# Kernel tuning notes

Hardware: AMD Instinct MI355X
Metric: run time of the kernel (lower is better)

The kernel has to match this reference:

```python
import jax, jax.numpy as jnp
import numpy as np

HIDDEN = 2048
N_HEADS = 32
N_KV_HEADS = 8
HEAD_DIM = HIDDEN // N_HEADS  # 64
N_GROUPS = N_HEADS // N_KV_HEADS  # 4
B, S = 1, 2048
NEG_INF = -1e9


def setup_inputs() -> dict:
    key = jax.random.key(0)
    k1, k2, k3, k4, k5 = jax.random.split(key, 5)
    hidden_states = jax.random.normal(k1, (B, S, HIDDEN), dtype=jnp.float32)
    # additive causal mask [B,1,S,S]
    causal = jnp.triu(jnp.full((S, S), NEG_INF, dtype=jnp.float32), k=1)
    attention_mask = jnp.broadcast_to(causal[None, None], (B, 1, S, S))
    position_ids = jnp.broadcast_to(jnp.arange(S, dtype=jnp.int32)[None], (B, S))
    scale = 0.02
    Wq = jax.random.normal(k2, (HIDDEN, N_HEADS * HEAD_DIM), dtype=jnp.float32) * scale
    Wk = jax.random.normal(k3, (HIDDEN, N_KV_HEADS * HEAD_DIM), dtype=jnp.float32) * scale
    Wv = jax.random.normal(k4, (HIDDEN, N_KV_HEADS * HEAD_DIM), dtype=jnp.float32) * scale
    Wo = jax.random.normal(k5, (HIDDEN, HIDDEN), dtype=jnp.float32) * scale
    return {"hidden_states": hidden_states, "attention_mask": attention_mask,
            "position_ids": position_ids, "Wq": Wq, "Wk": Wk, "Wv": Wv, "Wo": Wo}


def _rotate_half(x):
    x1, x2 = jnp.split(x, 2, axis=-1)
    return jnp.concatenate([-x2, x1], axis=-1)


def _rope_tables(kv_seq_len):
    inv_freq = 1.0 / (10000.0 ** (jnp.arange(0, HEAD_DIM, 2, dtype=jnp.float32) / HEAD_DIM))
    pos = jnp.arange(kv_seq_len, dtype=jnp.float32)
    freqs = pos[:, None] * inv_freq[None, :]          # [S, HD/2]
    emb = jnp.concatenate([freqs, freqs], axis=-1)    # [S, HD]
    return jnp.sin(emb), jnp.cos(emb)


def reference(hidden_states, attention_mask, position_ids, Wq, Wk, Wv, Wo):
    b, s, _ = hidden_states.shape
    q = (hidden_states @ Wq).reshape(b, s, N_HEADS, HEAD_DIM).transpose(0, 2, 1, 3)
    k = (hidden_states @ Wk).reshape(b, s, N_KV_HEADS, HEAD_DIM).transpose(0, 2, 1, 3)
    v = (hidden_states @ Wv).reshape(b, s, N_KV_HEADS, HEAD_DIM).transpose(0, 2, 1, 3)

    sin, cos = _rope_tables(s)
    cos_p = cos[position_ids][:, None]  # [B,1,S,HD]
    sin_p = sin[position_ids][:, None]
    q = q * cos_p + _rotate_half(q) * sin_p
    k = k * cos_p + _rotate_half(k) * sin_p

    # GQA: repeat_interleave kv heads along head axis
    k = jnp.repeat(k, N_GROUPS, axis=1)  # [B,H,S,HD]
    v = jnp.repeat(v, N_GROUPS, axis=1)

    q = q / jnp.sqrt(jnp.asarray(HEAD_DIM, q.dtype))
    scores = jnp.einsum('bhqd,bhkd->bhqk', q, k) + attention_mask
    attn = jax.nn.softmax(scores, axis=-1)
    out = jnp.einsum('bhqk,bhkd->bhqd', attn, v)
    out = out.transpose(0, 2, 1, 3).reshape(b, s, HIDDEN)
    return out @ Wo
```

## Files before the change

kernel.cpp:

```cpp
#include <hip/hip_runtime.h>
#include <hip/hip_bf16.h>

#define S_LEN 2048
#define HID 2048

typedef __attribute__((ext_vector_type(8))) short s16x8;
typedef __attribute__((ext_vector_type(4))) float f32x4;
typedef unsigned short u16;

__device__ __forceinline__ u16 f2bf(float f) {
  __hip_bfloat16 h = __float2bfloat16(f);
  return __builtin_bit_cast(u16, h);
}
__device__ __forceinline__ float bf2f(u16 u) {
  __hip_bfloat16 h = __builtin_bit_cast(__hip_bfloat16, u);
  return __bfloat162float(h);
}

#define GLD16(dst, src)                                                        \
  __builtin_amdgcn_global_load_lds(                                            \
      (__attribute__((address_space(1))) void*)(src),                          \
      (__attribute__((address_space(3))) void*)(dst), 16, 0, 0)

__global__ __launch_bounds__(256) void f2b_kernel(const float* __restrict__ in,
                                                  u16* __restrict__ outp, int n4) {
  int idx = blockIdx.x * 256 + threadIdx.x;
  if (idx >= n4) return;
  float4 v = *((const float4*)in + idx);
  ushort4 o;
  o.x = f2bf(v.x); o.y = f2bf(v.y); o.z = f2bf(v.z); o.w = f2bf(v.w);
  *((ushort4*)outp + idx) = o;
}

__global__ __launch_bounds__(256) void wtrans_kernel(const float* __restrict__ in,
                                                     u16* __restrict__ outp, int K, int N) {
  __shared__ u16 tile[32][33];
  int n0 = blockIdx.x * 32, k0 = blockIdx.y * 32;
  int tx = threadIdx.x & 31, ty = threadIdx.x >> 5;
#pragma unroll
  for (int r = 0; r < 4; ++r) {
    int row = ty + r * 8;
    tile[row][tx] = f2bf(in[(size_t)(k0 + row) * N + n0 + tx]);
  }
  __syncthreads();
#pragma unroll
  for (int r = 0; r < 4; ++r) {
    int row = ty + r * 8;
    outp[(size_t)(n0 + row) * K + k0 + tx] = tile[tx][row];
  }
}

__global__ __launch_bounds__(256) void wtransQKV_kernel(const float* __restrict__ Wq,
                                                        const float* __restrict__ Wk,
                                                        const float* __restrict__ Wv,
                                                        u16* __restrict__ outp) {
  __shared__ u16 tile[32][33];
  int n0g = blockIdx.x * 32, k0 = blockIdx.y * 32;
  const float* src;
  int n0, N;
  if (n0g < 2048)      { src = Wq; n0 = n0g;        N = 2048; }
  else if (n0g < 2560) { src = Wk; n0 = n0g - 2048; N = 512; }
  else                 { src = Wv; n0 = n0g - 2560; N = 512; }
  int tx = threadIdx.x & 31, ty = threadIdx.x >> 5;
#pragma unroll
  for (int r = 0; r < 4; ++r) {
    int row = ty + r * 8;
    tile[row][tx] = f2bf(src[(size_t)(k0 + row) * N + n0 + tx]);
  }
  __syncthreads();
#pragma unroll
  for (int r = 0; r < 4; ++r) {
    int row = ty + r * 8;
    outp[(size_t)(n0g + row) * HID + k0 + tx] = tile[tx][row];
  }
}

template <int MR, bool OUT_F32>
__global__ __launch_bounds__(256) void gemm_bt_kernel(const u16* __restrict__ A,
                                                      const u16* __restrict__ Bt,
                                                      void* __restrict__ C,
                                                      int M, int N, int K) {
  __shared__ u16 lA[MR * 1024];
  __shared__ u16 lB[128 * 32];
  int tid = threadIdx.x;
  int lane = tid & 63, w = tid >> 6;
  int lo = lane & 15, hi = lane >> 4;
  int wr = w >> 1, wc = w & 1;
  int brow = blockIdx.y * (MR * 32), bcol = blockIdx.x * 128;
  f32x4 z = {0.f, 0.f, 0.f, 0.f};
  f32x4 acc[MR][4];
#pragma unroll
  for (int m = 0; m < MR; ++m)
#pragma unroll
    for (int n = 0; n < 4; ++n) acc[m][n] = z;

  const u16* Abase = A + (size_t)brow * K;
  const u16* Bbase = Bt + (size_t)bcol * K;

  for (int k0 = 0; k0 < K; k0 += 32) {
#pragma unroll
    for (int r2 = 0; r2 < MR / 2; ++r2) {
      int c = r2 * 4 + w;
      GLD16(lA + c * 512, Abase + (size_t)(c * 16 + (lane >> 2)) * K + k0 + (lane & 3) * 8);
    }
#pragma unroll
    for (int r2 = 0; r2 < 2; ++r2) {
      int c = r2 * 4 + w;
      GLD16(lB + c * 512, Bbase + (size_t)(c * 16 + (lane >> 2)) * K + k0 + (lane & 3) * 8);
    }
    __syncthreads();
    s16x8 af[MR], bfr[4];
#pragma unroll
    for (int m = 0; m < MR; ++m)
      af[m] = *(const s16x8*)(lA + (wr * (MR * 16) + m * 16 + lo) * 32 + hi * 8);
#pragma unroll
    for (int n = 0; n < 4; ++n)
      bfr[n] = *(const s16x8*)(lB + (wc * 64 + n * 16 + lo) * 32 + hi * 8);
#pragma unroll
    for (int m = 0; m < MR; ++m)
#pragma unroll
      for (int n = 0; n < 4; ++n)
        acc[m][n] = __builtin_amdgcn_mfma_f32_16x16x32_bf16(af[m], bfr[n], acc[m][n], 0, 0, 0);
    __syncthreads();
  }
#pragma unroll
  for (int m = 0; m < MR; ++m)
#pragma unroll
    for (int n = 0; n < 4; ++n)
#pragma unroll
      for (int r = 0; r < 4; ++r) {
        int row = brow + wr * (MR * 16) + m * 16 + hi * 4 + r;
        int col = bcol + wc * 64 + n * 16 + lo;
        if (OUT_F32)
          ((float*)C)[(size_t)row * N + col] = acc[m][n][r];
        else
          ((u16*)C)[(size_t)row * N + col] = f2bf(acc[m][n][r]);
      }
}

__global__ __launch_bounds__(256) void rope_kernel(const u16* __restrict__ in,
                                                   u16* __restrict__ Qout,
                                                   u16* __restrict__ Kout,
                                                   const int* __restrict__ pos_ids) {
  int idx = blockIdx.x * 256 + threadIdx.x;
  int i = idx & 31;
  int t2 = idx >> 5;
  int hh, s;
  const u16* base;
  u16* outp;
  float scale;
  if (t2 < S_LEN * 32) {
    hh = t2 & 31; s = t2 >> 5;
    base = in + (size_t)s * 3072 + hh * 64;
    outp = Qout + ((size_t)hh * S_LEN + s) * 64;
    scale = 0.125f * 1.44269504f;
  } else {
    int t3 = t2 - S_LEN * 32;
    hh = t3 & 7; s = t3 >> 3;
    base = in + (size_t)s * 3072 + 2048 + hh * 64;
    outp = Kout + ((size_t)hh * S_LEN + s) * 64;
    scale = 1.0f;
  }
  float pos = (float)pos_ids[s];
  float inv = powf(10000.0f, -(float)(2 * i) / 64.0f);
  float ang = pos * inv;
  float c = cosf(ang), sn = sinf(ang);
  float q1 = bf2f(base[i]);
  float q2 = bf2f(base[i + 32]);
  outp[i] = f2bf((q1 * c - q2 * sn) * scale);
  outp[i + 32] = f2bf((q2 * c + q1 * sn) * scale);
}

__global__ __launch_bounds__(256) void vtrans_kernel(const u16* __restrict__ in,
                                                     u16* __restrict__ outp,
                                                     int in_stride, int in_off) {
  __shared__ u16 tile[32][33];
  int s0 = blockIdx.x * 32, d0 = blockIdx.y * 32;
  int tx = threadIdx.x & 31, ty = threadIdx.x >> 5;
#pragma unroll
  for (int r = 0; r < 4; ++r) {
    int row = ty + r * 8;
    tile[row][tx] = in[(size_t)(s0 + row) * in_stride + in_off + d0 + tx];
  }
  __syncthreads();
#pragma unroll
  for (int r = 0; r < 4; ++r) {
    int row = ty + r * 8;
    outp[(size_t)(d0 + row) * S_LEN + s0 + tx] = tile[tx][row];
  }
}

__global__ __launch_bounds__(512) void attn_kernel(const u16* __restrict__ Qr,
                                                   const u16* __restrict__ Kr,
                                                   const u16* __restrict__ Vt,
                                                   u16* __restrict__ AO) {
  __shared__ u16 lK[2][2][64 * 64];
  __shared__ u16 lV[2][2][64 * 64];
  __shared__ u16 lP[8][2][16 * 64];
  int g = blockIdx.x & 7;
  int p = blockIdx.x >> 3;
  int tid = threadIdx.x, lane = tid & 63, w = tid >> 6;
  int lo = lane & 15, hi = lane >> 4;
  int w2 = w >> 2;
  int h = g * 4 + (w & 3);
  int l8 = lane >> 3;
  int cs = ((lane & 7) ^ l8) * 8;

  const u16* Kbase = Kr + (size_t)g * S_LEN * 64;
  const u16* Vbase = Vt + (size_t)g * 64 * S_LEN;
  u16* Pw0 = &lP[w][0][0];
  u16* Pw1 = &lP[w][1][0];

#define STAGE_KV(buf, t)                                                                  \
  {                                                                                       \
    _Pragma("unroll") for (int hs = 0; hs < 2; ++hs) {                                    \
      GLD16(&lK[buf][hs][w * 512],                                                        \
            Kbase + ((size_t)((t) * 128 + hs * 64 + w * 8 + l8)) * 64 + cs);              \
      GLD16(&lV[buf][hs][w * 512],                                                        \
            Vbase + ((size_t)(w * 8 + l8)) * S_LEN + (t) * 128 + hs * 64 + cs);           \
    }                                                                                     \
  }

  f32x4 z = {0.f, 0.f, 0.f, 0.f};

#pragma unroll 1
  for (int pass = 0; pass < 2; ++pass) {
    int qt = pass ? p : 63 - p;
    int q0 = qt * 32;
    int tmax = (q0 + 31) >> 7;

    s16x8 aq[2];
    {
      const u16* qp = Qr + ((size_t)h * S_LEN + q0 + w2 * 16) * 64;
#pragma unroll
      for (int kk = 0; kk < 2; ++kk)
        aq[kk] = *(const s16x8*)(qp + (size_t)lo * 64 + kk * 32 + hi * 8);
    }

    f32x4 oacc[4];
#pragma unroll
    for (int n = 0; n < 4; ++n) oacc[n] = z;
    float mrun[4], ps[4];
#pragma unroll
    for (int r = 0; r < 4; ++r) { mrun[r] = -1e30f; ps[r] = 0.f; }

    int cur = 0;
    STAGE_KV(0, 0);
    __syncthreads();

    for (int t = 0; t <= tmax; ++t) {
      if (t < tmax) STAGE_KV(cur ^ 1, t + 1);

      f32x4 sacc[2][4];
#pragma unroll
      for (int hs = 0; hs < 2; ++hs)
#pragma unroll
        for (int n = 0; n < 4; ++n) sacc[hs][n] = z;
      __builtin_amdgcn_s_setprio(1);
#pragma unroll
      for (int hs = 0; hs < 2; ++hs)
#pragma unroll
        for (int kk = 0; kk < 2; ++kk)
#pragma unroll
          for (int n = 0; n < 4; ++n) {
            s16x8 bk = *(const s16x8*)(&lK[cur][hs][0] + (size_t)(n * 16 + lo) * 64 +
                                       ((kk * 4 + hi) ^ (lo & 7)) * 8);
            sacc[hs][n] = __builtin_amdgcn_mfma_f32_16x16x32_bf16(aq[kk], bk, sacc[hs][n], 0, 0, 0);
          }
      __builtin_amdgcn_s_setprio(0);

      if (t == tmax) {
#pragma unroll
        for (int hs = 0; hs < 2; ++hs)
#pragma unroll
          for (int n = 0; n < 4; ++n)
#pragma unroll
            for (int r = 0; r < 4; ++r) {
              int qg = q0 + w2 * 16 + hi * 4 + r;
              int kg = t * 128 + hs * 64 + n * 16 + lo;
              if (kg > qg) sacc[hs][n][r] = -1e30f;
            }
      }

      float tm[4];
#pragma unroll
      for (int r = 0; r < 4; ++r) {
        float a = fmaxf(fmaxf(sacc[0][0][r], sacc[0][1][r]), fmaxf(sacc[0][2][r], sacc[0][3][r]));
        float b = fmaxf(fmaxf(sacc[1][0][r], sacc[1][1][r]), fmaxf(sacc[1][2][r], sacc[1][3][r]));
        tm[r] = fmaxf(a, b);
      }
#pragma unroll
      for (int off = 1; off < 16; off <<= 1)
#pragma unroll
        for (int r = 0; r < 4; ++r) tm[r] = fmaxf(tm[r], __shfl_xor(tm[r], off, 64));

      float growth = -1e30f;
#pragma unroll
      for (int r = 0; r < 4; ++r) growth = fmaxf(growth, tm[r] - mrun[r]);
      if (__any(growth > 12.f)) {
#pragma unroll
        for (int r = 0; r < 4; ++r) {
          float nm = fmaxf(mrun[r], tm[r]);
          float scl = __builtin_amdgcn_exp2f(mrun[r] - nm);
          mrun[r] = nm;
          ps[r] *= scl;
#pragma unroll
          for (int n = 0; n < 4; ++n) oacc[n][r] *= scl;
        }
      }
#pragma unroll
      for (int hs = 0; hs < 2; ++hs)
#pragma unroll
        for (int n = 0; n < 4; ++n)
#pragma unroll
          for (int r = 0; r < 4; ++r)
            sacc[hs][n][r] = __builtin_amdgcn_exp2f(sacc[hs][n][r] - mrun[r]);
#pragma unroll
      for (int r = 0; r < 4; ++r)
        ps[r] += sacc[0][0][r] + sacc[0][1][r] + sacc[0][2][r] + sacc[0][3][r] +
                 sacc[1][0][r] + sacc[1][1][r] + sacc[1][2][r] + sacc[1][3][r];

#pragma unroll
      for (int r = 0; r < 4; ++r) {
        int row = hi * 4 + r;
#pragma unroll
        for (int n = 0; n < 4; ++n) {
          int col = (n * 16 + lo) ^ ((row & 7) * 8);
          Pw0[row * 64 + col] = f2bf(sacc[0][n][r]);
          Pw1[row * 64 + col] = f2bf(sacc[1][n][r]);
        }
      }

      __builtin_amdgcn_s_setprio(1);
#pragma unroll
      for (int hs = 0; hs < 2; ++hs) {
        const u16* Ph = hs ? Pw1 : Pw0;
#pragma unroll
        for (int kk = 0; kk < 2; ++kk) {
          s16x8 ap = *(const s16x8*)(Ph + (size_t)lo * 64 + ((kk * 4 + hi) ^ (lo & 7)) * 8);
#pragma unroll
          for (int n = 0; n < 4; ++n) {
            s16x8 bv = *(const s16x8*)(&lV[cur][hs][0] + (size_t)(n * 16 + lo) * 64 +
                                       ((kk * 4 + hi) ^ (lo & 7)) * 8);
            oacc[n] = __builtin_amdgcn_mfma_f32_16x16x32_bf16(ap, bv, oacc[n], 0, 0, 0);
          }
        }
      }
      __builtin_amdgcn_s_setprio(0);

      __syncthreads();
      cur ^= 1;
    }

#pragma unroll
    for (int off = 1; off < 16; off <<= 1)
#pragma unroll
      for (int r = 0; r < 4; ++r) ps[r] += __shfl_xor(ps[r], off, 64);

#pragma unroll
    for (int n = 0; n < 4; ++n)
#pragma unroll
      for (int r = 0; r < 4; ++r) {
        int q = q0 + w2 * 16 + hi * 4 + r;
        int d = n * 16 + lo;
        AO[(size_t)q * HID + h * 64 + d] = f2bf(oacc[n][r] / ps[r]);
      }
  }
#undef STAGE_KV
}

extern "C" void kernel_launch(void* const* d_in, const int* in_sizes, int n_in,
                              void* d_out, int out_size, void* d_ws, size_t ws_size,
                              hipStream_t stream) {
  const float* X  = (const float*)d_in[0];
  const int*   pos = (const int*)d_in[2];
  const float* Wq = (const float*)d_in[3];
  const float* Wk = (const float*)d_in[4];
  const float* Wv = (const float*)d_in[5];
  const float* Wo = (const float*)d_in[6];
  float* out = (float*)d_out;

  u16* Xb    = (u16*)d_ws;
  u16* WQKVt = Xb + (size_t)HID * HID;
  u16* Kr    = WQKVt;
  u16* Vt    = WQKVt + (size_t)8 * S_LEN * 64;
  u16* Wot   = WQKVt + (size_t)16 * S_LEN * 64;
  u16* QKVp  = WQKVt + (size_t)3072 * HID;
  u16* Qr    = Xb;
  u16* AO    = QKVp;

  f2b_kernel<<<(S_LEN * HID / 4 + 255) / 256, 256, 0, stream>>>(X, Xb, S_LEN * HID / 4);
  wtransQKV_kernel<<<dim3(3072 / 32, HID / 32), 256, 0, stream>>>(Wq, Wk, Wv, WQKVt);

  gemm_bt_kernel<2, false><<<dim3(3072 / 128, S_LEN / 64), 256, 0, stream>>>(Xb, WQKVt, QKVp, S_LEN, 3072, HID);

  rope_kernel<<<(S_LEN * 40 * 32) / 256, 256, 0, stream>>>(QKVp, Qr, Kr, pos);
  vtrans_kernel<<<dim3(S_LEN / 32, 512 / 32), 256, 0, stream>>>(QKVp, Vt, 3072, 2560);
  wtrans_kernel<<<dim3(HID / 32, HID / 32), 256, 0, stream>>>(Wo, Wot, HID, HID);

  attn_kernel<<<dim3(256), 512, 0, stream>>>(Qr, Kr, Vt, AO);

  gemm_bt_kernel<2, true><<<dim3(HID / 128, S_LEN / 64), 256, 0, stream>>>(AO, Wot, out, S_LEN, HID, HID);
}
```

Baseline: 268.0 us.

## Double-buffer GEMM with swizzled LDS, XCD-aware block mapping, split attention passes

The GEMM now uses 64-wide K steps with double-buffered, XOR-swizzled LDS staging. This overlaps global loads with MFMA work and reduces bank conflicts. Blocks are remapped across groups of eight so neighbouring tiles land on the same XCD for L2 reuse. The attention kernel drops its two-pass causal load balancing and launches one block per query tile (512 blocks), reusing a single P buffer per wave. The RoPE frequency is computed with exp2f instead of powf, which may shift rounding slightly.

```diff
diff --git a/kernel.cpp b/kernel.cpp
--- a/kernel.cpp
+++ b/kernel.cpp
@@ -75,61 +75,89 @@
   }
 }
 
-template <int MR, bool OUT_F32>
+template <bool OUT_F32>
 __global__ __launch_bounds__(256) void gemm_bt_kernel(const u16* __restrict__ A,
                                                       const u16* __restrict__ Bt,
                                                       void* __restrict__ C,
-                                                      int M, int N, int K) {
-  __shared__ u16 lA[MR * 1024];
-  __shared__ u16 lB[128 * 32];
+                                                      int N, int K, int sx) {
+  __shared__ u16 lA[2][64 * 64];
+  __shared__ u16 lB[2][128 * 64];
   int tid = threadIdx.x;
   int lane = tid & 63, w = tid >> 6;
   int lo = lane & 15, hi = lane >> 4;
   int wr = w >> 1, wc = w & 1;
-  int brow = blockIdx.y * (MR * 32), bcol = blockIdx.x * 128;
+  int blk = blockIdx.x;
+  int j = blk & 7, q = blk >> 3;
+  int bx = j * sx + (q % sx);
+  int by = q / sx;
+  int brow = by * 64, bcol = bx * 128;
+  int l8 = lane >> 3;
+  int cs = ((lane & 7) ^ l8) * 8;
+
   f32x4 z = {0.f, 0.f, 0.f, 0.f};
-  f32x4 acc[MR][4];
-#pragma unroll
-  for (int m = 0; m < MR; ++m)
+  f32x4 acc[2][4];
+#pragma unroll
+  for (int m = 0; m < 2; ++m)
 #pragma unroll
     for (int n = 0; n < 4; ++n) acc[m][n] = z;
 
   const u16* Abase = A + (size_t)brow * K;
   const u16* Bbase = Bt + (size_t)bcol * K;
 
-  for (int k0 = 0; k0 < K; k0 += 32) {
-#pragma unroll
-    for (int r2 = 0; r2 < MR / 2; ++r2) {
-      int c = r2 * 4 + w;
-      GLD16(lA + c * 512, Abase + (size_t)(c * 16 + (lane >> 2)) * K + k0 + (lane & 3) * 8);
-    }
-#pragma unroll
-    for (int r2 = 0; r2 < 2; ++r2) {
-      int c = r2 * 4 + w;
-      GLD16(lB + c * 512, Bbase + (size_t)(c * 16 + (lane >> 2)) * K + k0 + (lane & 3) * 8);
-    }
+#define GSTAGE(buf, k0)                                                                   \
+  {                                                                                       \
+    _Pragma("unroll") for (int r2 = 0; r2 < 2; ++r2) {                                    \
+      int c = r2 * 4 + w;                                                                 \
+      GLD16(&lA[buf][c * 512], Abase + (size_t)(c * 8 + l8) * K + (k0) + cs);             \
+    }                                                                                     \
+    _Pragma("unroll") for (int r2 = 0; r2 < 4; ++r2) {                                    \
+      int c = r2 * 4 + w;                                                                 \
+      GLD16(&lB[buf][c * 512], Bbase + (size_t)(c * 8 + l8) * K + (k0) + cs);             \
+    }                                                                                     \
+  }
+
+  int nsteps = K >> 6;
+  int cur = 0;
+  GSTAGE(0, 0);
+  __syncthreads();
+
+  for (int t = 0; t < nsteps; ++t) {
+    if (t + 1 < nsteps) GSTAGE(cur ^ 1, (t + 1) * 64);
+
+    s16x8 af[2][2], bfr[4][2];
+#pragma unroll
+    for (int m = 0; m < 2; ++m)
+#pragma unroll
+      for (int kk = 0; kk < 2; ++kk)
+        af[m][kk] = *(const s16x8*)(&lA[cur][0] + (size_t)(wr * 32 + m * 16 + lo) * 64 +
+                                    ((kk * 4 + hi) ^ (lo & 7)) * 8);
+#pragma unroll
+    for (int n = 0; n < 4; ++n)
+#pragma unroll
+      for (int kk = 0; kk < 2; ++kk)
+        bfr[n][kk] = *(const s16x8*)(&lB[cur][0] + (size_t)(wc * 64 + n * 16 + lo) * 64 +
+                                     ((kk * 4 + hi) ^ (lo & 7)) * 8);
+    __builtin_amdgcn_s_setprio(1);
+#pragma unroll
+    for (int kk = 0; kk < 2; ++kk)
+#pragma unroll
+      for (int m = 0; m < 2; ++m)
+#pragma unroll
+        for (int n = 0; n < 4; ++n)
+          acc[m][n] = __builtin_amdgcn_mfma_f32_16x16x32_bf16(af[m][kk], bfr[n][kk], acc[m][n], 0, 0, 0);
+    __builtin_amdgcn_s_setprio(0);
     __syncthreads();
-    s16x8 af[MR], bfr[4];
-#pragma unroll
-    for (int m = 0; m < MR; ++m)
-      af[m] = *(const s16x8*)(lA + (wr * (MR * 16) + m * 16 + lo) * 32 + hi * 8);
+    cur ^= 1;
+  }
+#undef GSTAGE
+
+#pragma unroll
+  for (int m = 0; m < 2; ++m)
 #pragma unroll
     for (int n = 0; n < 4; ++n)
-      bfr[n] = *(const s16x8*)(lB + (wc * 64 + n * 16 + lo) * 32 + hi * 8);
-#pragma unroll
-    for (int m = 0; m < MR; ++m)
-#pragma unroll
-      for (int n = 0; n < 4; ++n)
-        acc[m][n] = __builtin_amdgcn_mfma_f32_16x16x32_bf16(af[m], bfr[n], acc[m][n], 0, 0, 0);
-    __syncthreads();
-  }
-#pragma unroll
-  for (int m = 0; m < MR; ++m)
-#pragma unroll
-    for (int n = 0; n < 4; ++n)
 #pragma unroll
       for (int r = 0; r < 4; ++r) {
-        int row = brow + wr * (MR * 16) + m * 16 + hi * 4 + r;
+        int row = brow + wr * 32 + m * 16 + hi * 4 + r;
         int col = bcol + wc * 64 + n * 16 + lo;
         if (OUT_F32)
           ((float*)C)[(size_t)row * N + col] = acc[m][n][r];
@@ -162,7 +190,7 @@
     scale = 1.0f;
   }
   float pos = (float)pos_ids[s];
-  float inv = powf(10000.0f, -(float)(2 * i) / 64.0f);
+  float inv = exp2f(-(float)i * (13.2877124f / 32.f));
   float ang = pos * inv;
   float c = cosf(ang), sn = sinf(ang);
   float q1 = bf2f(base[i]);
@@ -196,20 +224,21 @@
                                                    u16* __restrict__ AO) {
   __shared__ u16 lK[2][2][64 * 64];
   __shared__ u16 lV[2][2][64 * 64];
-  __shared__ u16 lP[8][2][16 * 64];
+  __shared__ u16 lP[8][16 * 64];
   int g = blockIdx.x & 7;
-  int p = blockIdx.x >> 3;
+  int qt = 63 - (blockIdx.x >> 3);
+  int q0 = qt * 32;
   int tid = threadIdx.x, lane = tid & 63, w = tid >> 6;
   int lo = lane & 15, hi = lane >> 4;
   int w2 = w >> 2;
   int h = g * 4 + (w & 3);
+  int tmax = (q0 + 31) >> 7;
   int l8 = lane >> 3;
   int cs = ((lane & 7) ^ l8) * 8;
 
   const u16* Kbase = Kr + (size_t)g * S_LEN * 64;
   const u16* Vbase = Vt + (size_t)g * 64 * S_LEN;
-  u16* Pw0 = &lP[w][0][0];
-  u16* Pw1 = &lP[w][1][0];
+  u16* Pw = &lP[w][0];
 
 #define STAGE_KV(buf, t)                                                                  \
   {                                                                                       \
@@ -223,149 +252,139 @@
 
   f32x4 z = {0.f, 0.f, 0.f, 0.f};
 
-#pragma unroll 1
-  for (int pass = 0; pass < 2; ++pass) {
-    int qt = pass ? p : 63 - p;
-    int q0 = qt * 32;
-    int tmax = (q0 + 31) >> 7;
-
-    s16x8 aq[2];
-    {
-      const u16* qp = Qr + ((size_t)h * S_LEN + q0 + w2 * 16) * 64;
+  s16x8 aq[2];
+  {
+    const u16* qp = Qr + ((size_t)h * S_LEN + q0 + w2 * 16) * 64;
+#pragma unroll
+    for (int kk = 0; kk < 2; ++kk)
+      aq[kk] = *(const s16x8*)(qp + (size_t)lo * 64 + kk * 32 + hi * 8);
+  }
+
+  f32x4 oacc[4];
+#pragma unroll
+  for (int n = 0; n < 4; ++n) oacc[n] = z;
+  float mrun[4], ps[4];
+#pragma unroll
+  for (int r = 0; r < 4; ++r) { mrun[r] = -1e30f; ps[r] = 0.f; }
+
+  int cur = 0;
+  STAGE_KV(0, 0);
+  __syncthreads();
+
+  for (int t = 0; t <= tmax; ++t) {
+    if (t < tmax) STAGE_KV(cur ^ 1, t + 1);
+
+    f32x4 sacc[2][4];
+#pragma unroll
+    for (int hs = 0; hs < 2; ++hs)
+#pragma unroll
+      for (int n = 0; n < 4; ++n) sacc[hs][n] = z;
+    __builtin_amdgcn_s_setprio(1);
+#pragma unroll
+    for (int hs = 0; hs < 2; ++hs)
 #pragma unroll
       for (int kk = 0; kk < 2; ++kk)
-        aq[kk] = *(const s16x8*)(qp + (size_t)lo * 64 + kk * 32 + hi * 8);
+#pragma unroll
+        for (int n = 0; n < 4; ++n) {
+          s16x8 bk = *(const s16x8*)(&lK[cur][hs][0] + (size_t)(n * 16 + lo) * 64 +
+                                     ((kk * 4 + hi) ^ (lo & 7)) * 8);
+          sacc[hs][n] = __builtin_amdgcn_mfma_f32_16x16x32_bf16(aq[kk], bk, sacc[hs][n], 0, 0, 0);
+        }
+    __builtin_amdgcn_s_setprio(0);
+
+    if (t == tmax) {
+#pragma unroll
+      for (int hs = 0; hs < 2; ++hs)
+#pragma unroll
+        for (int n = 0; n < 4; ++n)
+#pragma unroll
+          for (int r = 0; r < 4; ++r) {
+            int qg = q0 + w2 * 16 + hi * 4 + r;
+            int kg = t * 128 + hs * 64 + n * 16 + lo;
+            if (kg > qg) sacc[hs][n][r] = -1e30f;
+          }
     }
 
-    f32x4 oacc[4];
-#pragma unroll
-    for (int n = 0; n < 4; ++n) oacc[n] = z;
-    float mrun[4], ps[4];
-#pragma unroll
-    for (int r = 0; r < 4; ++r) { mrun[r] = -1e30f; ps[r] = 0.f; }
-
-    int cur = 0;
-    STAGE_KV(0, 0);
-    __syncthreads();
-
-    for (int t = 0; t <= tmax; ++t) {
-      if (t < tmax) STAGE_KV(cur ^ 1, t + 1);
-
-      f32x4 sacc[2][4];
-#pragma unroll
-      for (int hs = 0; hs < 2; ++hs)
-#pragma unroll
-        for (int n = 0; n < 4; ++n) sacc[hs][n] = z;
-      __builtin_amdgcn_s_setprio(1);
-#pragma unroll
-      for (int hs = 0; hs < 2; ++hs)
-#pragma unroll
-        for (int kk = 0; kk < 2; ++kk)
-#pragma unroll
-          for (int n = 0; n < 4; ++n) {
-            s16x8 bk = *(const s16x8*)(&lK[cur][hs][0] + (size_t)(n * 16 + lo) * 64 +
-                                       ((kk * 4 + hi) ^ (lo & 7)) * 8);
-            sacc[hs][n] = __builtin_amdgcn_mfma_f32_16x16x32_bf16(aq[kk], bk, sacc[hs][n], 0, 0, 0);
-          }
-      __builtin_amdgcn_s_setprio(0);
-
-      if (t == tmax) {
-#pragma unroll
-        for (int hs = 0; hs < 2; ++hs)
-#pragma unroll
-          for (int n = 0; n < 4; ++n)
-#pragma unroll
-            for (int r = 0; r < 4; ++r) {
-              int qg = q0 + w2 * 16 + hi * 4 + r;
-              int kg = t * 128 + hs * 64 + n * 16 + lo;
-              if (kg > qg) sacc[hs][n][r] = -1e30f;
-            }
+    float tm[4];
+#pragma unroll
+    for (int r = 0; r < 4; ++r) {
+      float a = fmaxf(fmaxf(sacc[0][0][r], sacc[0][1][r]), fmaxf(sacc[0][2][r], sacc[0][3][r]));
+      float b = fmaxf(fmaxf(sacc[1][0][r], sacc[1][1][r]), fmaxf(sacc[1][2][r], sacc[1][3][r]));
+      tm[r] = fmaxf(a, b);
+    }
+#pragma unroll
+    for (int off = 1; off < 16; off <<= 1)
+#pragma unroll
+      for (int r = 0; r < 4; ++r) tm[r] = fmaxf(tm[r], __shfl_xor(tm[r], off, 64));
+
+    float growth = -1e30f;
+#pragma unroll
+    for (int r = 0; r < 4; ++r) growth = fmaxf(growth, tm[r] - mrun[r]);
+    if (__any(growth > 12.f)) {
+#pragma unroll
+      for (int r = 0; r < 4; ++r) {
+        float nm = fmaxf(mrun[r], tm[r]);
+        float scl = __builtin_amdgcn_exp2f(mrun[r] - nm);
+        mrun[r] = nm;
+        ps[r] *= scl;
+#pragma unroll
+        for (int n = 0; n < 4; ++n) oacc[n][r] *= scl;
       }
-
-      float tm[4];
+    }
+#pragma unroll
+    for (int hs = 0; hs < 2; ++hs)
+#pragma unroll
+      for (int n = 0; n < 4; ++n)
+#pragma unroll
+        for (int r = 0; r < 4; ++r)
+          sacc[hs][n][r] = __builtin_amdgcn_exp2f(sacc[hs][n][r] - mrun[r]);
+#pragma unroll
+    for (int r = 0; r < 4; ++r)
+      ps[r] += sacc[0][0][r] + sacc[0][1][r] + sacc[0][2][r] + sacc[0][3][r] +
+               sacc[1][0][r] + sacc[1][1][r] + sacc[1][2][r] + sacc[1][3][r];
+
+#pragma unroll
+    for (int hs = 0; hs < 2; ++hs) {
 #pragma unroll
       for (int r = 0; r < 4; ++r) {
-        float a = fmaxf(fmaxf(sacc[0][0][r], sacc[0][1][r]), fmaxf(sacc[0][2][r], sacc[0][3][r]));
-        float b = fmaxf(fmaxf(sacc[1][0][r], sacc[1][1][r]), fmaxf(sacc[1][2][r], sacc[1][3][r]));
-        tm[r] = fmaxf(a, b);
-      }
-#pragma unroll
-      for (int off = 1; off < 16; off <<= 1)
-#pragma unroll
-        for (int r = 0; r < 4; ++r) tm[r] = fmaxf(tm[r], __shfl_xor(tm[r], off, 64));
-
-      float growth = -1e30f;
-#pragma unroll
-      for (int r = 0; r < 4; ++r) growth = fmaxf(growth, tm[r] - mrun[r]);
-      if (__any(growth > 12.f)) {
-#pragma unroll
-        for (int r = 0; r < 4; ++r) {
-          float nm = fmaxf(mrun[r], tm[r]);
-          float scl = __builtin_amdgcn_exp2f(mrun[r] - nm);
-          mrun[r] = nm;
-          ps[r] *= scl;
-#pragma unroll
-          for (int n = 0; n < 4; ++n) oacc[n][r] *= scl;
+        int row = hi * 4 + r;
+#pragma unroll
+        for (int n = 0; n < 4; ++n) {
+          int col = (n * 16 + lo) ^ ((row & 7) * 8);
+          Pw[row * 64 + col] = f2bf(sacc[hs][n][r]);
         }
       }
-#pragma unroll
-      for (int hs = 0; hs < 2; ++hs)
-#pragma unroll
-        for (int n = 0; n < 4; ++n)
-#pragma unroll
-          for (int r = 0; r < 4; ++r)
-            sacc[hs][n][r] = __builtin_amdgcn_exp2f(sacc[hs][n][r] - mrun[r]);
-#pragma unroll
-      for (int r = 0; r < 4; ++r)
-        ps[r] += sacc[0][0][r] + sacc[0][1][r] + sacc[0][2][r] + sacc[0][3][r] +
-                 sacc[1][0][r] + sacc[1][1][r] + sacc[1][2][r] + sacc[1][3][r];
-
-#pragma unroll
-      for (int r = 0; r < 4; ++r) {
-        int row = hi * 4 + r;
+      __builtin_amdgcn_s_setprio(1);
+#pragma unroll
+      for (int kk = 0; kk < 2; ++kk) {
+        s16x8 ap = *(const s16x8*)(Pw + (size_t)lo * 64 + ((kk * 4 + hi) ^ (lo & 7)) * 8);
 #pragma unroll
         for (int n = 0; n < 4; ++n) {
-          int col = (n * 16 + lo) ^ ((row & 7) * 8);
-          Pw0[row * 64 + col] = f2bf(sacc[0][n][r]);
-          Pw1[row * 64 + col] = f2bf(sacc[1][n][r]);
-        }
-      }
-
-      __builtin_amdgcn_s_setprio(1);
-#pragma unroll
-      for (int hs = 0; hs < 2; ++hs) {
-        const u16* Ph = hs ? Pw1 : Pw0;
-#pragma unroll
-        for (int kk = 0; kk < 2; ++kk) {
-          s16x8 ap = *(const s16x8*)(Ph + (size_t)lo * 64 + ((kk * 4 + hi) ^ (lo & 7)) * 8);
-#pragma unroll
-          for (int n = 0; n < 4; ++n) {
-            s16x8 bv = *(const s16x8*)(&lV[cur][hs][0] + (size_t)(n * 16 + lo) * 64 +
-                                       ((kk * 4 + hi) ^ (lo & 7)) * 8);
-            oacc[n] = __builtin_amdgcn_mfma_f32_16x16x32_bf16(ap, bv, oacc[n], 0, 0, 0);
-          }
+          s16x8 bv = *(const s16x8*)(&lV[cur][hs][0] + (size_t)(n * 16 + lo) * 64 +
+                                     ((kk * 4 + hi) ^ (lo & 7)) * 8);
+          oacc[n] = __builtin_amdgcn_mfma_f32_16x16x32_bf16(ap, bv, oacc[n], 0, 0, 0);
         }
       }
       __builtin_amdgcn_s_setprio(0);
-
-      __syncthreads();
-      cur ^= 1;
     }
 
-#pragma unroll
-    for (int off = 1; off < 16; off <<= 1)
-#pragma unroll
-      for (int r = 0; r < 4; ++r) ps[r] += __shfl_xor(ps[r], off, 64);
-
-#pragma unroll
-    for (int n = 0; n < 4; ++n)
-#pragma unroll
-      for (int r = 0; r < 4; ++r) {
-        int q = q0 + w2 * 16 + hi * 4 + r;
-        int d = n * 16 + lo;
-        AO[(size_t)q * HID + h * 64 + d] = f2bf(oacc[n][r] / ps[r]);
-      }
-  }
+    __syncthreads();
+    cur ^= 1;
+  }
+
+#pragma unroll
+  for (int off = 1; off < 16; off <<= 1)
+#pragma unroll
+    for (int r = 0; r < 4; ++r) ps[r] += __shfl_xor(ps[r], off, 64);
+
+#pragma unroll
+  for (int n = 0; n < 4; ++n)
+#pragma unroll
+    for (int r = 0; r < 4; ++r) {
+      int q = q0 + w2 * 16 + hi * 4 + r;
+      int d = n * 16 + lo;
+      AO[(size_t)q * HID + h * 64 + d] = f2bf(oacc[n][r] / ps[r]);
+    }
 #undef STAGE_KV
 }
 
@@ -392,13 +411,14 @@
   f2b_kernel<<<(S_LEN * HID / 4 + 255) / 256, 256, 0, stream>>>(X, Xb, S_LEN * HID / 4);
   wtransQKV_kernel<<<dim3(3072 / 32, HID / 32), 256, 0, stream>>>(Wq, Wk, Wv, WQKVt);
 
-  gemm_bt_kernel<2, false><<<dim3(3072 / 128, S_LEN / 64), 256, 0, stream>>>(Xb, WQKVt, QKVp, S_LEN, 3072, HID);
+  gemm_bt_kernel<false><<<dim3(768), 256, 0, stream>>>(Xb, WQKVt, QKVp, 3072, HID, 3);
+
+  wtrans_kernel<<<dim3(HID / 32, HID / 32), 256, 0, stream>>>(Wo, Wot, HID, HID);
 
   rope_kernel<<<(S_LEN * 40 * 32) / 256, 256, 0, stream>>>(QKVp, Qr, Kr, pos);
   vtrans_kernel<<<dim3(S_LEN / 32, 512 / 32), 256, 0, stream>>>(QKVp, Vt, 3072, 2560);
-  wtrans_kernel<<<dim3(HID / 32, HID / 32), 256, 0, stream>>>(Wo, Wot, HID, HID);
-
-  attn_kernel<<<dim3(256), 512, 0, stream>>>(Qr, Kr, Vt, AO);
-
-  gemm_bt_kernel<2, true><<<dim3(HID / 128, S_LEN / 64), 256, 0, stream>>>(AO, Wot, out, S_LEN, HID, HID);
-}
+
+  attn_kernel<<<dim3(512), 512, 0, stream>>>(Qr, Kr, Vt, AO);
+
+  gemm_bt_kernel<true><<<dim3(512), 256, 0, stream>>>(AO, Wot, out, HID, HID, 2);
+}
```

New measurement: 240.3 us. -10.3%, faster.
